# Kernel tuning notes

Measured on AMD Instinct MI355X. Metric: run time of the kernel, lower is better.

## Reference

```python
import jax, jax.numpy as jnp
import numpy as np

N_NODES = 10000
N_EDGES = 640000
D_IN = 128
D_OUT = 128


def setup_inputs() -> dict:
    key = jax.random.key(0)
    k_x, k_val, k_w, k_row, k_col = jax.random.split(key, 5)
    # Glorot init for weight, zeros for bias (matches _weight_init)
    limit = float(np.sqrt(6.0 / (D_IN + D_OUT)))
    weight = jax.random.uniform(k_w, (D_IN, D_OUT), jnp.float32, -limit, limit)
    return {
        "x": jax.random.normal(k_x, (N_NODES, D_IN), jnp.float32),
        "adj_val": jax.random.uniform(k_val, (N_EDGES,), jnp.float32),  # normalized edge weights of sparse adj
        "weight": weight,
        "bias": jnp.zeros((D_OUT,), jnp.float32),
        "adj_row": jax.random.randint(k_row, (N_EDGES,), 0, N_NODES, jnp.int32),
        "adj_col": jax.random.randint(k_col, (N_EDGES,), 0, N_NODES, jnp.int32),
    }


def reference(x, adj_val, weight, bias, adj_row, adj_col):
    # dense GEMM: h = x @ W  -> [N, D_OUT]
    h = jnp.matmul(x, weight)
    # SpMM with COO adjacency: out[r] = sum_{e: row[e]=r} val[e] * h[col[e]]
    msg = adj_val[:, None] * h[adj_col]  # [E, D_OUT] gather + scale
    out = jax.ops.segment_sum(msg, adj_row, num_segments=x.shape[0])
    return out + bias
```

## Files before the change

kernel.cpp:

```cpp
#include <hip/hip_runtime.h>

#define N_NODES 10000
#define N_EDGES 640000
#define D 128

#define GRID1 1024
#define GEMM_BLOCKS 157
#define SCAT_BLOCKS (GRID1 - GEMM_BLOCKS)
#define CAP 32
#define OVF_CAP 8192
#define LSTR 136
#define QPAD 272

typedef unsigned int uint32;
typedef unsigned short u16;
using short8 = __attribute__((ext_vector_type(8))) short;
using f32x4  = __attribute__((ext_vector_type(4))) float;

__device__ __forceinline__ uint32 f2bf_bits(float f) {
    uint32 u = __float_as_uint(f);
    return (u + 0x7FFFu + ((u >> 16) & 1u)) >> 16;
}
__device__ __forceinline__ uint32 pack2(float lo, float hi) {
    return f2bf_bits(lo) | (f2bf_bits(hi) << 16);
}

__device__ __forceinline__ void scat_one(int r, uint32 rc, int s,
                                         int* __restrict__ cursor,
                                         uint32* __restrict__ region,
                                         int* ovf_cnt, uint2* ovf)
{
    int pos = atomicAdd(&cursor[s * N_NODES + r], 1);
    if (pos < CAP) {
        region[(r * 8 + s) * CAP + pos] = rc;
    } else {
        int o = atomicAdd(ovf_cnt, 1);
        if (o < OVF_CAP) ovf[o] = make_uint2((uint32)r, rc);
    }
}

__global__ __launch_bounds__(256, 4) void gemm_scatter_kernel(
    const float* __restrict__ x, const float* __restrict__ w,
    const int* __restrict__ row, const int* __restrict__ col,
    const float* __restrict__ val,
    uint32* __restrict__ h2, int* __restrict__ cursor,
    int* __restrict__ ovf_cnt, uint2* __restrict__ ovf,
    uint32* __restrict__ region)
{
    __shared__ __align__(16) u16 Ws[128 * LSTR];
    const int t = threadIdx.x;
    const int lane = t & 63;
    const int wid  = t >> 6;

    if (blockIdx.x < GEMM_BLOCKS) {
        const int q = lane >> 4, cl = lane & 15;

        #pragma unroll
        for (int i = 0; i < 32; ++i) {
            int lin = t + i * 256;
            int c = lin & 127;
            int m = lin >> 7;
            float w0 = w[(2 * m) * D + c];
            float w1 = w[(2 * m + 1) * D + c];
            *(uint32*)&Ws[c * LSTR + 2 * m] = pack2(w0, w1);
        }

        int gr = blockIdx.x * 64 + wid * 16 + cl;
        if (gr >= N_NODES) gr = N_NODES - 1;
        const float* xrow = &x[(size_t)gr * D];
        float4 xv[8];
        #pragma unroll
        for (int kk = 0; kk < 4; ++kk) {
            xv[2 * kk]     = *(const float4*)&xrow[kk * 32 + q * 8];
            xv[2 * kk + 1] = *(const float4*)&xrow[kk * 32 + q * 8 + 4];
        }
        __syncthreads();

        f32x4 acc[8] = {};
        #pragma unroll
        for (int kk = 0; kk < 4; ++kk) {
            union { short8 s; uint32 u[4]; } af;
            float4 a = xv[2 * kk], b = xv[2 * kk + 1];
            af.u[0] = pack2(a.x, a.y); af.u[1] = pack2(a.z, a.w);
            af.u[2] = pack2(b.x, b.y); af.u[3] = pack2(b.z, b.w);
            #pragma unroll
            for (int ct = 0; ct < 8; ++ct) {
                short8 bf = *(const short8*)&Ws[(ct * 16 + cl) * LSTR + kk * 32 + q * 8];
                acc[ct] = __builtin_amdgcn_mfma_f32_16x16x32_bf16(af.s, bf, acc[ct], 0, 0, 0);
            }
        }
        #pragma unroll
        for (int reg = 0; reg < 4; ++reg) {
            int node = blockIdx.x * 64 + wid * 16 + q * 4 + reg;
            if (node < N_NODES) {
                uint32* base = h2 + (size_t)node * 64 + cl;
                #pragma unroll
                for (int ct = 0; ct < 4; ++ct)
                    base[ct * 16] = pack2(acc[ct][reg], acc[ct + 4][reg]);
            }
        }
    } else {
        const int xcc = blockIdx.x & 7;
        const int tid    = (blockIdx.x - GEMM_BLOCKS) * 256 + t;
        const int stride = SCAT_BLOCKS * 256;
        const int4*   row4 = (const int4*)row;
        const int4*   col4 = (const int4*)col;
        const float4* val4 = (const float4*)val;
        for (int i = tid; i < N_EDGES / 4; i += stride) {
            int4 r = row4[i]; int4 c = col4[i]; float4 v = val4[i];
            scat_one(r.x, (uint32)c.x | (f2bf_bits(v.x) << 16), xcc, cursor, region, ovf_cnt, ovf);
            scat_one(r.y, (uint32)c.y | (f2bf_bits(v.y) << 16), xcc, cursor, region, ovf_cnt, ovf);
            scat_one(r.z, (uint32)c.z | (f2bf_bits(v.z) << 16), xcc, cursor, region, ovf_cnt, ovf);
            scat_one(r.w, (uint32)c.w | (f2bf_bits(v.w) << 16), xcc, cursor, region, ovf_cnt, ovf);
        }
    }
}

__global__ __launch_bounds__(256) void spmm_kernel(
    const uint32* __restrict__ region, const int* __restrict__ cursor,
    const int* __restrict__ ovf_cnt, const uint2* __restrict__ ovf,
    const uint32* __restrict__ h2, const float* __restrict__ bias,
    float* __restrict__ out)
{
    __shared__ uint32 qbuf[4 * QPAD];
    const int t = threadIdx.x;
    const int lane = t & 63;
    const int wid  = t >> 6;
    const int r = blockIdx.x * 4 + wid;
    uint32* qb = &qbuf[wid * QPAD];

    uint32 rl[4];
    #pragma unroll
    for (int i = 0; i < 4; ++i)
        rl[i] = region[r * 256 + i * 64 + lane];

    int ns[8], pref[9];
    pref[0] = 0;
    #pragma unroll
    for (int s = 0; s < 8; ++s) {
        int c = cursor[s * N_NODES + r];
        ns[s] = (c < CAP) ? c : CAP;
        pref[s + 1] = pref[s] + ns[s];
    }
    const int ntot = pref[8];

    #pragma unroll
    for (int i = 0; i < 4; ++i) {
        int p  = lane & 31;
        int hi = lane >> 5;
        int n_  = hi ? ns[2 * i + 1]   : ns[2 * i];
        int pf  = hi ? pref[2 * i + 1] : pref[2 * i];
        if (p < n_) qb[pf + p] = rl[i];
    }
    if (lane < 16) qb[ntot + lane] = 0;
    __builtin_amdgcn_s_waitcnt(0);

    const int npad = (ntot + 7) & ~7;
    float a0 = 0.f, a1 = 0.f;

    uint32 rq0,rq1,rq2,rq3,rq4,rq5,rq6,rq7;
    uint32 hh0,hh1,hh2,hh3,hh4,hh5,hh6,hh7;
    rq0 = qb[0]; hh0 = h2[((rq0 & 0xFFFFu) << 6) + lane];
    rq1 = qb[1]; hh1 = h2[((rq1 & 0xFFFFu) << 6) + lane];
    rq2 = qb[2]; hh2 = h2[((rq2 & 0xFFFFu) << 6) + lane];
    rq3 = qb[3]; hh3 = h2[((rq3 & 0xFFFFu) << 6) + lane];
    rq4 = qb[4]; hh4 = h2[((rq4 & 0xFFFFu) << 6) + lane];
    rq5 = qb[5]; hh5 = h2[((rq5 & 0xFFFFu) << 6) + lane];
    rq6 = qb[6]; hh6 = h2[((rq6 & 0xFFFFu) << 6) + lane];
    rq7 = qb[7]; hh7 = h2[((rq7 & 0xFFFFu) << 6) + lane];

#define CONSUME_PREFETCH(RQ, HH, P)                                          \
    {                                                                        \
        a0 = fmaf(__uint_as_float(RQ & 0xFFFF0000u),                         \
                  __uint_as_float(HH << 16), a0);                            \
        a1 = fmaf(__uint_as_float(RQ & 0xFFFF0000u),                         \
                  __uint_as_float(HH & 0xFFFF0000u), a1);                    \
        uint32 rn = qb[j + 8 + P];                                           \
        RQ = rn; HH = h2[((rn & 0xFFFFu) << 6) + lane];                      \
    }

    for (int j = 0; j < npad; j += 8) {
        CONSUME_PREFETCH(rq0, hh0, 0)
        CONSUME_PREFETCH(rq1, hh1, 1)
        CONSUME_PREFETCH(rq2, hh2, 2)
        CONSUME_PREFETCH(rq3, hh3, 3)
        CONSUME_PREFETCH(rq4, hh4, 4)
        CONSUME_PREFETCH(rq5, hh5, 5)
        CONSUME_PREFETCH(rq6, hh6, 6)
        CONSUME_PREFETCH(rq7, hh7, 7)
    }
#undef CONSUME_PREFETCH

    int novf = ovf_cnt[0];
    if (novf > OVF_CAP) novf = OVF_CAP;
    for (int k = 0; k < novf; ++k) {
        uint2 e = ovf[k];
        if (e.x == (uint32)r) {
            uint32 qq = e.y;
            uint32 hv = h2[((qq & 0xFFFFu) << 6) + lane];
            a0 = fmaf(__uint_as_float(qq & 0xFFFF0000u), __uint_as_float(hv << 16), a0);
            a1 = fmaf(__uint_as_float(qq & 0xFFFF0000u), __uint_as_float(hv & 0xFFFF0000u), a1);
        }
    }

    out[(size_t)r * D + lane]      = a0 + bias[lane];
    out[(size_t)r * D + 64 + lane] = a1 + bias[lane + 64];
}

extern "C" void kernel_launch(void* const* d_in, const int* in_sizes, int n_in,
                              void* d_out, int out_size, void* d_ws, size_t ws_size,
                              hipStream_t stream)
{
    const float* x    = (const float*)d_in[0];
    const float* aval = (const float*)d_in[1];
    const float* w    = (const float*)d_in[2];
    const float* bias = (const float*)d_in[3];
    const int* arow   = (const int*)d_in[4];
    const int* acol   = (const int*)d_in[5];

    char* ws = (char*)d_ws;
    uint32* h2     = (uint32*)(ws);
    int*    cursor = (int*)(ws + 2560000);
    int*    ovfcnt = (int*)(ws + 2880000);
    uint2*  ovf    = (uint2*)(ws + 2880064);
    uint32* region = (uint32*)(ws + 2945600);

    hipMemsetAsync(ws + 2560000, 0, 320004, stream);

    gemm_scatter_kernel<<<GRID1, 256, 0, stream>>>(
        x, w, arow, acol, aval, h2, cursor, ovfcnt, ovf, region);
    spmm_kernel<<<N_NODES / 4, 256, 0, stream>>>(
        region, cursor, ovfcnt, ovf, h2, bias, (float*)d_out);
}
```

Before: 115.9 us.

## Replace per-row atomic scatter with block-local bucketed counting sort of edges

Edges are now binned into coarse 128-row buckets. Each scatter block first counts its edges per bucket in LDS, then reserves a range in each bucket with one global atomic per bucket, then writes (col|val, row) pairs into that range. This removes the per-edge global atomics and shrinks the zeroing memset from about 320KB of per-row cursors to a few hundred bytes. In exchange, every SpMM block scans its whole bucket (thousands of entries) to pull out its 4 rows through LDS atomics, which adds heavy, redundant L2 traffic. The grid is also halved, and overflow entries pushed during the SpMM kernel can race with other blocks that are reading the overflow list.

```diff
diff --git a/kernel.cpp b/kernel.cpp
--- a/kernel.cpp
+++ b/kernel.cpp
@@ -3,16 +3,20 @@
 #define N_NODES 10000
 #define N_EDGES 640000
 #define D 128
-
-#define GRID1 1024
+#define NQ (N_EDGES / 4)
+
+#define GRID1 512
 #define GEMM_BLOCKS 157
 #define SCAT_BLOCKS (GRID1 - GEMM_BLOCKS)
-#define CAP 32
+#define NBUCK 79
+#define BCAP 10240
+#define CAP2 128
+#define QPAD2 144
 #define OVF_CAP 8192
 #define LSTR 136
-#define QPAD 272
 
 typedef unsigned int uint32;
+typedef unsigned long long u64;
 typedef unsigned short u16;
 using short8 = __attribute__((ext_vector_type(8))) short;
 using f32x4  = __attribute__((ext_vector_type(4))) float;
@@ -25,27 +29,20 @@
     return f2bf_bits(lo) | (f2bf_bits(hi) << 16);
 }
 
-__device__ __forceinline__ void scat_one(int r, uint32 rc, int s,
-                                         int* __restrict__ cursor,
-                                         uint32* __restrict__ region,
-                                         int* ovf_cnt, uint2* ovf)
-{
-    int pos = atomicAdd(&cursor[s * N_NODES + r], 1);
-    if (pos < CAP) {
-        region[(r * 8 + s) * CAP + pos] = rc;
-    } else {
-        int o = atomicAdd(ovf_cnt, 1);
-        if (o < OVF_CAP) ovf[o] = make_uint2((uint32)r, rc);
-    }
+__device__ __forceinline__ void ovf_push(int r, uint32 rc, int* ovf_cnt, u64* ovf) {
+    int o = atomicAdd(ovf_cnt, 1);
+    if (o < OVF_CAP)
+        __hip_atomic_store(&ovf[o], ((u64)(uint32)r << 32) | rc,
+                           __ATOMIC_RELAXED, __HIP_MEMORY_SCOPE_AGENT);
 }
 
 __global__ __launch_bounds__(256, 4) void gemm_scatter_kernel(
     const float* __restrict__ x, const float* __restrict__ w,
     const int* __restrict__ row, const int* __restrict__ col,
     const float* __restrict__ val,
-    uint32* __restrict__ h2, int* __restrict__ cursor,
-    int* __restrict__ ovf_cnt, uint2* __restrict__ ovf,
-    uint32* __restrict__ region)
+    uint32* __restrict__ h2, int* __restrict__ gcnt,
+    int* __restrict__ ovf_cnt, u64* __restrict__ ovf,
+    uint2* __restrict__ bstore)
 {
     __shared__ __align__(16) u16 Ws[128 * LSTR];
     const int t = threadIdx.x;
@@ -100,58 +97,84 @@
             }
         }
     } else {
-        const int xcc = blockIdx.x & 7;
-        const int tid    = (blockIdx.x - GEMM_BLOCKS) * 256 + t;
-        const int stride = SCAT_BLOCKS * 256;
+        int* lcnt  = (int*)Ws;
+        int* lbase = (int*)Ws + 96;
+        int* lcnt2 = (int*)Ws + 192;
+        if (t < NBUCK) lcnt[t] = 0;
+        __syncthreads();
+
+        const int sb = blockIdx.x - GEMM_BLOCKS;
         const int4*   row4 = (const int4*)row;
         const int4*   col4 = (const int4*)col;
         const float4* val4 = (const float4*)val;
-        for (int i = tid; i < N_EDGES / 4; i += stride) {
+
+        for (int i = sb * 256 + t; i < NQ; i += SCAT_BLOCKS * 256) {
+            int4 r = row4[i];
+            atomicAdd(&lcnt[r.x >> 7], 1);
+            atomicAdd(&lcnt[r.y >> 7], 1);
+            atomicAdd(&lcnt[r.z >> 7], 1);
+            atomicAdd(&lcnt[r.w >> 7], 1);
+        }
+        __syncthreads();
+        if (t < NBUCK) {
+            int c = lcnt[t];
+            lbase[t] = (c > 0) ? atomicAdd(&gcnt[t], c) : 0;
+            lcnt2[t] = 0;
+        }
+        __syncthreads();
+
+        for (int i = sb * 256 + t; i < NQ; i += SCAT_BLOCKS * 256) {
             int4 r = row4[i]; int4 c = col4[i]; float4 v = val4[i];
-            scat_one(r.x, (uint32)c.x | (f2bf_bits(v.x) << 16), xcc, cursor, region, ovf_cnt, ovf);
-            scat_one(r.y, (uint32)c.y | (f2bf_bits(v.y) << 16), xcc, cursor, region, ovf_cnt, ovf);
-            scat_one(r.z, (uint32)c.z | (f2bf_bits(v.z) << 16), xcc, cursor, region, ovf_cnt, ovf);
-            scat_one(r.w, (uint32)c.w | (f2bf_bits(v.w) << 16), xcc, cursor, region, ovf_cnt, ovf);
+            #pragma unroll
+            for (int e = 0; e < 4; ++e) {
+                int rr = (e == 0) ? r.x : (e == 1) ? r.y : (e == 2) ? r.z : r.w;
+                int cc = (e == 0) ? c.x : (e == 1) ? c.y : (e == 2) ? c.z : c.w;
+                float vv = (e == 0) ? v.x : (e == 1) ? v.y : (e == 2) ? v.z : v.w;
+                uint32 rc = (uint32)cc | (f2bf_bits(vv) << 16);
+                int b = rr >> 7;
+                int k = atomicAdd(&lcnt2[b], 1);
+                int pos = lbase[b] + k;
+                if (pos < BCAP)
+                    bstore[(size_t)b * BCAP + pos] = make_uint2(rc, (uint32)rr);
+                else
+                    ovf_push(rr, rc, ovf_cnt, ovf);
+            }
         }
     }
 }
 
 __global__ __launch_bounds__(256) void spmm_kernel(
-    const uint32* __restrict__ region, const int* __restrict__ cursor,
-    const int* __restrict__ ovf_cnt, const uint2* __restrict__ ovf,
+    const uint2* __restrict__ bstore, const int* __restrict__ gcnt,
+    int* __restrict__ ovf_cnt, u64* __restrict__ ovf,
     const uint32* __restrict__ h2, const float* __restrict__ bias,
     float* __restrict__ out)
 {
-    __shared__ uint32 qbuf[4 * QPAD];
+    __shared__ uint32 qbuf[4 * QPAD2];
+    __shared__ int cnt[4];
     const int t = threadIdx.x;
     const int lane = t & 63;
     const int wid  = t >> 6;
-    const int r = blockIdx.x * 4 + wid;
-    uint32* qb = &qbuf[wid * QPAD];
-
-    uint32 rl[4];
-    #pragma unroll
-    for (int i = 0; i < 4; ++i)
-        rl[i] = region[r * 256 + i * 64 + lane];
-
-    int ns[8], pref[9];
-    pref[0] = 0;
-    #pragma unroll
-    for (int s = 0; s < 8; ++s) {
-        int c = cursor[s * N_NODES + r];
-        ns[s] = (c < CAP) ? c : CAP;
-        pref[s + 1] = pref[s] + ns[s];
-    }
-    const int ntot = pref[8];
-
-    #pragma unroll
-    for (int i = 0; i < 4; ++i) {
-        int p  = lane & 31;
-        int hi = lane >> 5;
-        int n_  = hi ? ns[2 * i + 1]   : ns[2 * i];
-        int pf  = hi ? pref[2 * i + 1] : pref[2 * i];
-        if (p < n_) qb[pf + p] = rl[i];
-    }
+    const int r0 = blockIdx.x * 4;
+    const int b  = r0 >> 7;
+
+    if (t < 4) cnt[t] = 0;
+    __syncthreads();
+
+    int n = gcnt[b]; if (n > BCAP) n = BCAP;
+    for (int i = t; i < n; i += 256) {
+        uint2 e = bstore[(size_t)b * BCAP + i];
+        uint32 d = e.y - (uint32)r0;
+        if (d < 4u) {
+            int k = atomicAdd(&cnt[d], 1);
+            if (k < CAP2) qbuf[d * QPAD2 + k] = e.x;
+            else ovf_push((int)e.y, e.x, ovf_cnt, ovf);
+        }
+    }
+    __syncthreads();
+
+    const int r = r0 + wid;
+    uint32* qb = &qbuf[wid * QPAD2];
+    int ntot = cnt[wid]; if (ntot > CAP2) ntot = CAP2;
     if (lane < 16) qb[ntot + lane] = 0;
     __builtin_amdgcn_s_waitcnt(0);
 
@@ -191,12 +214,12 @@
     }
 #undef CONSUME_PREFETCH
 
-    int novf = ovf_cnt[0];
+    int novf = __hip_atomic_load(ovf_cnt, __ATOMIC_RELAXED, __HIP_MEMORY_SCOPE_AGENT);
     if (novf > OVF_CAP) novf = OVF_CAP;
     for (int k = 0; k < novf; ++k) {
-        uint2 e = ovf[k];
-        if (e.x == (uint32)r) {
-            uint32 qq = e.y;
+        u64 e = __hip_atomic_load(&ovf[k], __ATOMIC_RELAXED, __HIP_MEMORY_SCOPE_AGENT);
+        if ((uint32)(e >> 32) == (uint32)r) {
+            uint32 qq = (uint32)e;
             uint32 hv = h2[((qq & 0xFFFFu) << 6) + lane];
             a0 = fmaf(__uint_as_float(qq & 0xFFFF0000u), __uint_as_float(hv << 16), a0);
             a1 = fmaf(__uint_as_float(qq & 0xFFFF0000u), __uint_as_float(hv & 0xFFFF0000u), a1);
@@ -220,15 +243,15 @@
 
     char* ws = (char*)d_ws;
     uint32* h2     = (uint32*)(ws);
-    int*    cursor = (int*)(ws + 2560000);
-    int*    ovfcnt = (int*)(ws + 2880000);
-    uint2*  ovf    = (uint2*)(ws + 2880064);
-    uint32* region = (uint32*)(ws + 2945600);
-
-    hipMemsetAsync(ws + 2560000, 0, 320004, stream);
+    int*    gcnt   = (int*)(ws + 2560000);
+    int*    ovfcnt = (int*)(ws + 2560320);
+    u64*    ovf    = (u64*)(ws + 2560384);
+    uint2*  bstore = (uint2*)(ws + 2625920);
+
+    hipMemsetAsync(ws + 2560000, 0, 324, stream);
 
     gemm_scatter_kernel<<<GRID1, 256, 0, stream>>>(
-        x, w, arow, acol, aval, h2, cursor, ovfcnt, ovf, region);
+        x, w, arow, acol, aval, h2, gcnt, ovfcnt, ovf, bstore);
     spmm_kernel<<<N_NODES / 4, 256, 0, stream>>>(
-        region, cursor, ovfcnt, ovf, h2, bias, (float*)d_out);
-}
+        bstore, gcnt, ovfcnt, ovf, h2, bias, (float*)d_out);
+}
```

Measured after the change: 121.7 us. +5.1%, slower.
